# Performance work log

Measured on AMD Instinct MI355X. Metric: run time of the kernel, lower is better.

The kernel has to match this reference:

```python
import jax, jax.numpy as jnp
import numpy as np
import math

EMBED = 512
KDIM = 512
VDIM = 512
H = 8
HD = EMBED // H
N = 2048
L = 2048
B = 4


def setup_inputs() -> dict:
    key = jax.random.key(0)
    ks = jax.random.split(key, 14)
    s = 1.0 / math.sqrt(EMBED)
    return {
        "q": jax.random.normal(ks[0], (N, B, EMBED), jnp.float32),
        "k": jax.random.normal(ks[1], (L, B, KDIM), jnp.float32),
        "v": jax.random.normal(ks[2], (L, B, VDIM), jnp.float32),
        "pe1": jax.random.normal(ks[3], (B, N, 3), jnp.float32),
        "pe2": jax.random.normal(ks[4], (L, 3), jnp.float32),
        "Wq": jax.random.normal(ks[5], (EMBED, EMBED), jnp.float32) * s,
        "bq": jnp.zeros((EMBED,), jnp.float32),
        "Wk": jax.random.normal(ks[6], (EMBED, KDIM), jnp.float32) * s,
        "bk": jnp.zeros((EMBED,), jnp.float32),
        "Wv": jax.random.normal(ks[7], (EMBED, VDIM), jnp.float32) * s,
        "bv": jnp.zeros((EMBED,), jnp.float32),
        "Wo": jax.random.normal(ks[8], (EMBED, EMBED), jnp.float32) * s,
        "bo": jnp.zeros((EMBED,), jnp.float32),
    }


def reference(q, k, v, pe1, pe2, Wq, bq, Wk, bk, Wv, bv, Wo, bo):
    n, b, _ = q.shape
    l = k.shape[0]
    # projections (nn.Linear: x @ W.T + b)
    qp = q @ Wq.T + bq  # (n, b, E)
    kp = k @ Wk.T + bk  # (l, b, E)
    vp = v @ Wv.T + bv  # (l, b, E)
    # split heads -> (b, H, n, hd)
    qh = qp.reshape(n, b, H, HD).transpose(1, 2, 0, 3)
    kh = kp.reshape(l, b, H, HD).transpose(1, 2, 0, 3)
    vh = vp.reshape(l, b, H, HD).transpose(1, 2, 0, 3)
    # relative PE bias: (b, n, l), broadcast over heads
    pe_scores = jnp.einsum('bnc,lc->bnl', pe1, pe2)[:, None, :, :]
    scores = (jnp.einsum('bhnd,bhld->bhnl', qh, kh) + pe_scores) / math.sqrt(HD)
    attn = jax.nn.softmax(scores, axis=-1)
    out = jnp.einsum('bhnl,bhld->bhnd', attn, vh)  # (b, H, n, hd)
    out = out.transpose(2, 0, 1, 3).reshape(n, b, EMBED)
    return out @ Wo.T + bo
```

## Files before the change

### kernel.cpp

```cpp
#include <hip/hip_runtime.h>
#include <math.h>

#define EMBED 512
#define HDIM 64
#define NHEADS 8
#define SEQ_N 2048
#define SEQ_L 2048
#define BATCH 4
#define MROWS (SEQ_N*BATCH)
#define BE (BATCH*EMBED)

#define QSCALE 0.18033688f

typedef _Float16 f16;
typedef _Float16 half8 __attribute__((ext_vector_type(8)));
typedef _Float16 half4 __attribute__((ext_vector_type(4)));
typedef _Float16 half2v __attribute__((ext_vector_type(2)));
typedef float floatx4 __attribute__((ext_vector_type(4)));
typedef float floatx16 __attribute__((ext_vector_type(16)));

static __device__ inline float fast_exp2(float x) {
#if __has_builtin(__builtin_amdgcn_exp2f)
  return __builtin_amdgcn_exp2f(x);
#else
  return __expf(x * 0.69314718056f);
#endif
}

static __device__ inline half2v pk2(float a, float b) {
#if __has_builtin(__builtin_amdgcn_cvt_pkrtz)
  return __builtin_bit_cast(half2v, __builtin_amdgcn_cvt_pkrtz(a, b));
#else
  half2v o; o[0] = (f16)a; o[1] = (f16)b; return o;
#endif
}

static __device__ inline half8 cvt8(float4 u, float4 v) {
  half2v p0 = pk2(u.x, u.y), p1 = pk2(u.z, u.w);
  half2v p2 = pk2(v.x, v.y), p3 = pk2(v.z, v.w);
  half8 o;
  o[0] = p0[0]; o[1] = p0[1]; o[2] = p1[0]; o[3] = p1[1];
  o[4] = p2[0]; o[5] = p2[1]; o[6] = p3[0]; o[7] = p3[1];
  return o;
}

static __device__ inline void gload16(const void* g, void* l) {
  __builtin_amdgcn_global_load_lds(
      (__attribute__((address_space(1))) void*)(g),
      (__attribute__((address_space(3))) void*)(l), 16, 0, 0);
}

__global__ __launch_bounds__(256) void cvt_w(const float* __restrict__ Wq,
                                             const float* __restrict__ Wk,
                                             const float* __restrict__ Wv,
                                             const float* __restrict__ Wo,
                                             f16* __restrict__ Wb) {
  const long WSZ = (long)EMBED * EMBED;
  long i = ((long)blockIdx.x * 256 + threadIdx.x) * 4;
  int sel = (int)(i >> 18);
  long off = i & (WSZ - 1);
  const float* s = sel == 0 ? Wq : sel == 1 ? Wk : sel == 2 ? Wv : Wo;
  float4 f = *reinterpret_cast<const float4*>(s + off);
  half4 o; o[0] = (f16)f.x; o[1] = (f16)f.y; o[2] = (f16)f.z; o[3] = (f16)f.w;
  *reinterpret_cast<half4*>(Wb + i) = o;
}

__global__ __launch_bounds__(256) void gemm_qkv(const float* __restrict__ A0,
                                                const float* __restrict__ A1,
                                                const float* __restrict__ A2,
                                                const f16* __restrict__ W0,
                                                const f16* __restrict__ W1,
                                                const f16* __restrict__ W2,
                                                const float* __restrict__ b0,
                                                const float* __restrict__ b1,
                                                const float* __restrict__ b2,
                                                f16* __restrict__ C0, f16* __restrict__ C1,
                                                f16* __restrict__ C2t) {
  __shared__ alignas(16) unsigned char gsm[34816];
  f16* As = reinterpret_cast<f16*>(gsm);
  f16* Bs = reinterpret_cast<f16*>(gsm + 16384);
  f16* T  = reinterpret_cast<f16*>(gsm);
  const int sel = blockIdx.y >> 2;
  const float* A = sel == 0 ? A0 : sel == 1 ? A1 : A2;
  const f16* Bt = sel == 0 ? W0 : sel == 1 ? W1 : W2;
  const float* bias = sel == 0 ? b0 : sel == 1 ? b1 : b2;
  const float scl = sel == 0 ? QSCALE : 1.0f;
  const int tid = threadIdx.x;
  const int wave = tid >> 6, lane = tid & 63, quad = lane >> 4, l16 = lane & 15;
  const int wm = wave & 1, wn = wave >> 1;
  const long m0 = (long)blockIdx.x * 128;
  const long n0 = (long)(blockIdx.y & 3) * 128;
  const int srow = lane >> 2;
  const int scol = (lane & 3) * 8;

  const int ar = tid >> 1;
  const int ah = (tid & 1) * 16;
  const float* Agp = A + (m0 + ar) * EMBED + ah;
  const f16* Bg0 = Bt + (n0 + wave * 32 + srow) * EMBED + scol;
  const f16* Bg1 = Bt + (n0 + wave * 32 + 16 + srow) * EMBED + scol;

  {
    float4 a4[4];
#pragma unroll
    for (int j = 0; j < 4; ++j)
      a4[j] = *reinterpret_cast<const float4*>(Agp + j * 4);
    gload16(Bg0, &Bs[(wave * 32) * 32]);
    gload16(Bg1, &Bs[(wave * 32 + 16) * 32]);
    *reinterpret_cast<half8*>(&As[ar * 32 + ah]) = cvt8(a4[0], a4[1]);
    *reinterpret_cast<half8*>(&As[ar * 32 + ah + 8]) = cvt8(a4[2], a4[3]);
  }
  floatx4 acc[4][4] = {};
  __syncthreads();

#pragma unroll
  for (int ks = 0; ks < 16; ++ks) {
    const int cur = ks & 1;
    float4 a4[4];
    if (ks + 1 < 16) {
      const int k1 = (ks + 1) * 32;
#pragma unroll
      for (int j = 0; j < 4; ++j)
        a4[j] = *reinterpret_cast<const float4*>(Agp + k1 + j * 4);
      gload16(Bg0 + k1, &Bs[(cur ^ 1) * 4096 + (wave * 32) * 32]);
      gload16(Bg1 + k1, &Bs[(cur ^ 1) * 4096 + (wave * 32 + 16) * 32]);
    }
    half8 af[4], bf[4];
#pragma unroll
    for (int i = 0; i < 4; ++i)
      af[i] = *reinterpret_cast<const half8*>(&As[cur * 4096 + (wm * 64 + i * 16 + l16) * 32 + quad * 8]);
#pragma unroll
    for (int j = 0; j < 4; ++j)
      bf[j] = *reinterpret_cast<const half8*>(&Bs[cur * 4096 + (wn * 64 + j * 16 + l16) * 32 + quad * 8]);
#pragma unroll
    for (int i = 0; i < 4; ++i)
#pragma unroll
      for (int j = 0; j < 4; ++j)
        acc[i][j] = __builtin_amdgcn_mfma_f32_16x16x32_f16(af[i], bf[j], acc[i][j], 0, 0, 0);
    if (ks + 1 < 16) {
      *reinterpret_cast<half8*>(&As[(cur ^ 1) * 4096 + ar * 32 + ah]) = cvt8(a4[0], a4[1]);
      *reinterpret_cast<half8*>(&As[(cur ^ 1) * 4096 + ar * 32 + ah + 8]) = cvt8(a4[2], a4[3]);
      __syncthreads();
    }
  }

  if (sel != 2) {
    f16* C = sel == 0 ? C0 : C1;
#pragma unroll
    for (int i = 0; i < 4; ++i)
#pragma unroll
      for (int r = 0; r < 4; ++r) {
        long row = m0 + wm * 64 + i * 16 + quad * 4 + r;
#pragma unroll
        for (int j = 0; j < 4; ++j) {
          long col = n0 + wn * 64 + j * 16 + l16;
          float val = (acc[i][j][r] + bias[col]) * scl;
          C[row * EMBED + col] = (f16)val;
        }
      }
  } else {
    __syncthreads();
#pragma unroll
    for (int i = 0; i < 4; ++i)
#pragma unroll
      for (int r = 0; r < 4; ++r) {
        int mrow = wm * 64 + i * 16 + quad * 4 + r;
        int bq = mrow & 3, lt = mrow >> 2;
#pragma unroll
        for (int j = 0; j < 4; ++j) {
          int col = wn * 64 + j * 16 + l16;
          float val = acc[i][j][r] + bias[n0 + col];
          T[col * 136 + bq * 32 + lt] = (f16)val;
        }
      }
    __syncthreads();
    const int h0 = (int)(n0 >> 6);
    const long lbase = m0 >> 2;
#pragma unroll
    for (int it = 0; it < 8; ++it) {
      int f = it * 256 + tid;
      int ls = f & 3, bq = (f >> 2) & 3, d6 = (f >> 4) & 63, hl = f >> 10;
      half8 o = *reinterpret_cast<const half8*>(&T[(hl * 64 + d6) * 136 + bq * 32 + ls * 8]);
      *reinterpret_cast<half8*>(C2t + (((long)bq * 8 + h0 + hl) * 64 + d6) * 2048 + lbase + ls * 8) = o;
    }
  }
}

__global__ __launch_bounds__(256) void gemm_out(const f16* __restrict__ A,
                                                const f16* __restrict__ Bt,
                                                const float* __restrict__ bias,
                                                float* __restrict__ C) {
  __shared__ alignas(16) f16 As[2][128 * 32];
  __shared__ alignas(16) f16 Bs[2][64 * 32];
  const int tid = threadIdx.x;
  const int wave = tid >> 6, lane = tid & 63, quad = lane >> 4, l16 = lane & 15;
  const long m0 = (long)blockIdx.x * 128;
  const long n0 = (long)blockIdx.y * 64;
  const int srow = lane >> 2;
  const int scol = (lane & 3) * 8;

  const f16* Ag0 = A + (m0 + wave * 32 + srow) * EMBED + scol;
  const f16* Ag1 = A + (m0 + wave * 32 + 16 + srow) * EMBED + scol;
  const f16* Bg0 = Bt + (n0 + wave * 16 + srow) * EMBED + scol;

  gload16(Ag0, &As[0][(wave * 32) * 32]);
  gload16(Ag1, &As[0][(wave * 32 + 16) * 32]);
  gload16(Bg0, &Bs[0][(wave * 16) * 32]);
  floatx4 acc[2][4] = {};
  asm volatile("s_waitcnt vmcnt(0)" ::: "memory");
  __builtin_amdgcn_s_barrier();

#pragma unroll
  for (int ks = 0; ks < 16; ++ks) {
    const int cur = ks & 1;
    if (ks + 1 < 16) {
      const int k1 = (ks + 1) * 32;
      gload16(Ag0 + k1, &As[cur ^ 1][(wave * 32) * 32]);
      gload16(Ag1 + k1, &As[cur ^ 1][(wave * 32 + 16) * 32]);
      gload16(Bg0 + k1, &Bs[cur ^ 1][(wave * 16) * 32]);
    }
    half8 af[2], bf[4];
#pragma unroll
    for (int i = 0; i < 2; ++i)
      af[i] = *reinterpret_cast<const half8*>(&As[cur][(wave * 32 + i * 16 + l16) * 32 + quad * 8]);
#pragma unroll
    for (int j = 0; j < 4; ++j)
      bf[j] = *reinterpret_cast<const half8*>(&Bs[cur][(j * 16 + l16) * 32 + quad * 8]);
#pragma unroll
    for (int i = 0; i < 2; ++i)
#pragma unroll
      for (int j = 0; j < 4; ++j)
        acc[i][j] = __builtin_amdgcn_mfma_f32_16x16x32_f16(af[i], bf[j], acc[i][j], 0, 0, 0);
    if (ks + 1 < 16) {
      asm volatile("s_waitcnt vmcnt(0)" ::: "memory");
      __builtin_amdgcn_s_barrier();
    }
  }
#pragma unroll
  for (int i = 0; i < 2; ++i)
#pragma unroll
    for (int r = 0; r < 4; ++r) {
      long row = m0 + wave * 32 + i * 16 + quad * 4 + r;
#pragma unroll
      for (int j = 0; j < 4; ++j) {
        long col = n0 + j * 16 + l16;
        C[row * EMBED + col] = acc[i][j][r] + bias[col];
      }
    }
}

#define KBUFB (128 * 64 * 2)
#define VBUFB (64 * 128 * 2)
#define PEBUFB (128 * 16 * 2)
#define LDSB (2 * KBUFB + 2 * VBUFB + 2 * PEBUFB)
#define NCHUNK (SEQ_L / 128)
__global__ __launch_bounds__(512, 4) void attn_flash(const f16* __restrict__ qp,
                                                     const f16* __restrict__ kp,
                                                     const f16* __restrict__ vt,
                                                     const float* __restrict__ pe1,
                                                     const float* __restrict__ pe2,
                                                     f16* __restrict__ ao) {
  __shared__ alignas(16) unsigned char smem[LDSB];
  f16* K0 = reinterpret_cast<f16*>(smem);
  f16* V0 = reinterpret_cast<f16*>(smem + 2 * KBUFB);
  f16* P0 = reinterpret_cast<f16*>(smem + 2 * KBUFB + 2 * VBUFB);
  float* comb = reinterpret_cast<float*>(smem);
  const int tid = threadIdx.x, wave = tid >> 6, lane = tid & 63;
  const int m = lane & 31, h = lane >> 5;
  const int strip = wave & 3, half = wave >> 2;
  const int W = blockIdx.y * 16 + blockIdx.x;
  const int bh = (W & 7) + ((W >> 7) << 3);
  const int n0 = ((W >> 3) & 15) * 128;
  const int b = bh >> 3, hd = bh & 7;
  const long headoff = (long)b * EMBED + hd * HDIM;
  const long vhead = (long)bh * 64 * 2048;

  const int krow0 = wave * 16 + (lane >> 3);
  const int kg = (lane & 7) ^ (lane >> 3);
  const f16* ksrc0 = kp + headoff + (long)krow0 * BE + kg * 8;
  const int vd0 = wave * 8 + (lane >> 4);
  const int vd1 = vd0 + 4;
  const int vg0 = (lane & 15) ^ (vd0 & 7);
  const int vg1 = (lane & 15) ^ (vd1 & 7);
  const f16* vsrc0 = vt + vhead + (long)vd0 * 2048 + vg0 * 8;
  const f16* vsrc1 = vt + vhead + (long)vd1 * 2048 + vg1 * 8;

  for (int c = tid; c < 1024; c += 512) {
    int r = c >> 3, col = (c & 7) * 8;
    *reinterpret_cast<uint4*>(&K0[r * 64 + col]) =
        *reinterpret_cast<const uint4*>(qp + (long)(n0 + r) * BE + headoff + col);
  }
  gload16(vsrc0, V0 + wave * 1024);
  gload16(vsrc1, V0 + wave * 1024 + 512);
  if (tid < 256) {
    const uint2 z2 = {0, 0};
    const uint4 z4 = {0, 0, 0, 0};
    *reinterpret_cast<uint2*>(reinterpret_cast<char*>(P0) + tid * 32 + 8) = z2;
    *reinterpret_cast<uint4*>(reinterpret_cast<char*>(P0) + tid * 32 + 16) = z4;
  }
  if (tid < 128) {
    long base = ((long)b * SEQ_N + n0 + tid) * 3;
    half4 v8;
    v8[0] = (f16)(pe1[base + 0] * QSCALE);
    v8[1] = (f16)(pe1[base + 1] * QSCALE);
    v8[2] = (f16)(pe1[base + 2] * QSCALE);
    v8[3] = (f16)0.f;
    *reinterpret_cast<half4*>(&P0[tid * 16]) = v8;
  }
  __syncthreads();

  half8 qf[5];
#pragma unroll
  for (int e = 0; e < 4; ++e)
    qf[e] = *reinterpret_cast<const half8*>(&K0[(strip * 32 + m) * 64 + e * 16 + h * 8]);
  qf[4] = *reinterpret_cast<const half8*>(&P0[(strip * 32 + m) * 16 + h * 8]);
  __syncthreads();

  gload16(ksrc0, K0 + wave * 1024);
  gload16(ksrc0 + 8 * BE, K0 + wave * 1024 + 512);
  {
    int pr = tid & 127;
    float a0 = pe2[(long)pr * 3 + 0];
    float a1 = pe2[(long)pr * 3 + 1];
    float a2 = pe2[(long)pr * 3 + 2];
    if (tid < 128) {
      half4 p2v; p2v[0] = (f16)a0; p2v[1] = (f16)a1; p2v[2] = (f16)a2; p2v[3] = (f16)0.f;
      *reinterpret_cast<half4*>(&P0[tid * 16]) = p2v;
    }
  }
  __syncthreads();

  floatx16 oacc[2] = {};
  float lpart = 0.f;

  auto compute_chunk = [&](int bsel) {
    const f16* Kb = K0 + bsel * 8192;
    const f16* Vb = V0 + bsel * 8192;
    const f16* Pb = P0 + bsel * 2048;
#pragma unroll
    for (int tt = 0; tt < 2; ++tt) {
      const int t = half * 2 + tt;
      const int row = t * 32 + m;
      const int r7 = m & 7;
      floatx16 st = {};
#pragma unroll
      for (int e = 0; e < 4; ++e) {
        half8 kf = *reinterpret_cast<const half8*>(&Kb[row * 64 + (((2 * e + h) ^ r7) * 8)]);
        st = __builtin_amdgcn_mfma_f32_32x32x16_f16(kf, qf[e], st, 0, 0, 0);
      }
      {
        half8 kf = *reinterpret_cast<const half8*>(&Pb[row * 16 + h * 8]);
        st = __builtin_amdgcn_mfma_f32_32x32x16_f16(kf, qf[4], st, 0, 0, 0);
      }
      float p[16];
#pragma unroll
      for (int r = 0; r < 16; ++r) {
        p[r] = fast_exp2(st[r]);
        lpart += p[r];
      }
#pragma unroll
      for (int s = 0; s < 4; ++s) {
        half2v u0 = pk2(p[4 * s + 0], p[4 * s + 1]);
        half2v u1 = pk2(p[4 * s + 2], p[4 * s + 3]);
        half4 bp;
        bp[0] = u0[0]; bp[1] = u0[1]; bp[2] = u1[0]; bp[3] = u1[1];
        const int sl = t * 4 + s;
#pragma unroll
        for (int dt = 0; dt < 2; ++dt) {
          const int d = dt * 32 + m;
          half4 vf = *reinterpret_cast<const half4*>(&Vb[d * 128 + ((sl ^ r7) * 8) + h * 4]);
          oacc[dt] = __builtin_amdgcn_mfma_f32_32x32x8f16(vf, bp, oacc[dt], 0, 0, 0);
        }
      }
    }
  };

  int buf = 0;
#pragma unroll 1
  for (int c = 0; c < NCHUNK - 1; ++c) {
    const int l0n = (c + 1) * 128;
    f16* Kn = K0 + (buf ^ 1) * 8192;
    f16* Vn = V0 + (buf ^ 1) * 8192;
    gload16(ksrc0 + (long)l0n * BE, Kn + wave * 1024);
    gload16(ksrc0 + (long)l0n * BE + 8 * BE, Kn + wave * 1024 + 512);
    gload16(vsrc0 + l0n, Vn + wave * 1024);
    gload16(vsrc1 + l0n, Vn + wave * 1024 + 512);
    int pr = tid & 127;
    float a0 = pe2[(long)(l0n + pr) * 3 + 0];
    float a1 = pe2[(long)(l0n + pr) * 3 + 1];
    float a2 = pe2[(long)(l0n + pr) * 3 + 2];

    compute_chunk(buf);

    if (tid < 128) {
      half4 p2v; p2v[0] = (f16)a0; p2v[1] = (f16)a1; p2v[2] = (f16)a2; p2v[3] = (f16)0.f;
      *reinterpret_cast<half4*>(&P0[(buf ^ 1) * 2048 + tid * 16]) = p2v;
    }
    __syncthreads();
    buf ^= 1;
  }
  compute_chunk(buf);
  __syncthreads();

  lpart += __shfl_xor(lpart, 32);

  if (half == 1) {
    float* dst = comb + (strip * 64 + lane) * 33;
#pragma unroll
    for (int dt = 0; dt < 2; ++dt)
#pragma unroll
      for (int x = 0; x < 16; ++x) dst[dt * 16 + x] = oacc[dt][x];
    dst[32] = lpart;
  }
  __syncthreads();
  if (half == 0) {
    const float* src = comb + (strip * 64 + lane) * 33;
#pragma unroll
    for (int dt = 0; dt < 2; ++dt)
#pragma unroll
      for (int x = 0; x < 16; ++x) oacc[dt][x] += src[dt * 16 + x];
    float inv = 1.f / (lpart + src[32]);
    long qrow = n0 + strip * 32 + m;
#pragma unroll
    for (int dt = 0; dt < 2; ++dt)
#pragma unroll
      for (int g = 0; g < 4; ++g) {
        half4 o4;
#pragma unroll
        for (int x = 0; x < 4; ++x) o4[x] = (f16)(oacc[dt][4 * g + x] * inv);
        int d = dt * 32 + 8 * g + 4 * h;
        *reinterpret_cast<half4*>(ao + qrow * BE + headoff + d) = o4;
      }
  }
}

extern "C" void kernel_launch(void* const* d_in, const int* in_sizes, int n_in,
                              void* d_out, int out_size, void* d_ws, size_t ws_size,
                              hipStream_t stream) {
  const float* q   = (const float*)d_in[0];
  const float* k   = (const float*)d_in[1];
  const float* v   = (const float*)d_in[2];
  const float* pe1 = (const float*)d_in[3];
  const float* pe2 = (const float*)d_in[4];
  const float* Wq  = (const float*)d_in[5];
  const float* bq  = (const float*)d_in[6];
  const float* Wk  = (const float*)d_in[7];
  const float* bk  = (const float*)d_in[8];
  const float* Wv  = (const float*)d_in[9];
  const float* bv  = (const float*)d_in[10];
  const float* Wo  = (const float*)d_in[11];
  const float* bo  = (const float*)d_in[12];
  float* out = (float*)d_out;

  f16* ws = (f16*)d_ws;
  const long TOK = (long)MROWS * EMBED;
  const long WSZ = (long)EMBED * EMBED;
  f16* Wqb = ws;
  f16* Wkb = Wqb + WSZ;
  f16* Wvb = Wkb + WSZ;
  f16* Wob = Wvb + WSZ;
  f16* qpb = Wob + WSZ;
  f16* kpb = qpb + TOK;
  f16* vtb = kpb + TOK;
  f16* aob = vtb + TOK;

  cvt_w<<<dim3(1024), 256, 0, stream>>>(Wq, Wk, Wv, Wo, Wqb);

  gemm_qkv<<<dim3(MROWS / 128, 12), 256, 0, stream>>>(q, k, v, Wqb, Wkb, Wvb,
                                                      bq, bk, bv, qpb, kpb, vtb);

  attn_flash<<<dim3(SEQ_N / 128, BATCH * NHEADS), 512, 0, stream>>>(qpb, kpb, vtb, pe1, pe2, aob);

  gemm_out<<<dim3(MROWS / 128, EMBED / 64), 256, 0, stream>>>(aob, Wob, bo, out);
}
```

Baseline: 208.7 us.

## Stage fp32 A tiles via async LDS loads and use 32x32x16 MFMA for PV

The QKV projection now copies fp32 activation tiles straight into shared memory with async global-to-LDS loads, using an XOR-swizzled layout. It converts them to fp16 when it reads the MFMA fragments, so the register round trip and the separate convert-and-store step go away. In attention, the P·V product switches from 32x32x8 to 32x32x16 MFMA, using v_permlane32_swap to rearrange the packed probabilities into 8-wide fragments, which halves the MFMA instruction count. The costs are double the LDS footprint for A, which may reduce occupancy, and conversion work repeated per fragment read.

```diff
diff --git a/kernel.cpp b/kernel.cpp
--- a/kernel.cpp
+++ b/kernel.cpp
@@ -18,6 +18,7 @@
 typedef _Float16 half2v __attribute__((ext_vector_type(2)));
 typedef float floatx4 __attribute__((ext_vector_type(4)));
 typedef float floatx16 __attribute__((ext_vector_type(16)));
+typedef unsigned int uint4v __attribute__((ext_vector_type(4)));
 
 static __device__ inline float fast_exp2(float x) {
 #if __has_builtin(__builtin_amdgcn_exp2f)
@@ -76,9 +77,9 @@
                                                 const float* __restrict__ b2,
                                                 f16* __restrict__ C0, f16* __restrict__ C1,
                                                 f16* __restrict__ C2t) {
-  __shared__ alignas(16) unsigned char gsm[34816];
-  f16* As = reinterpret_cast<f16*>(gsm);
-  f16* Bs = reinterpret_cast<f16*>(gsm + 16384);
+  __shared__ alignas(16) unsigned char gsm[49152];
+  float* As = reinterpret_cast<float*>(gsm);
+  f16* Bs = reinterpret_cast<f16*>(gsm + 32768);
   f16* T  = reinterpret_cast<f16*>(gsm);
   const int sel = blockIdx.y >> 2;
   const float* A = sel == 0 ? A0 : sel == 1 ? A1 : A2;
@@ -93,41 +94,43 @@
   const int srow = lane >> 2;
   const int scol = (lane & 3) * 8;
 
-  const int ar = tid >> 1;
-  const int ah = (tid & 1) * 16;
-  const float* Agp = A + (m0 + ar) * EMBED + ah;
+  const int arow = lane >> 3;
+  const int aslot = (lane & 7) ^ arow;
+  const float* Agp = A + (m0 + wave * 32 + arow) * EMBED + aslot * 4;
   const f16* Bg0 = Bt + (n0 + wave * 32 + srow) * EMBED + scol;
   const f16* Bg1 = Bt + (n0 + wave * 32 + 16 + srow) * EMBED + scol;
 
-  {
-    float4 a4[4];
-#pragma unroll
-    for (int j = 0; j < 4; ++j)
-      a4[j] = *reinterpret_cast<const float4*>(Agp + j * 4);
-    gload16(Bg0, &Bs[(wave * 32) * 32]);
-    gload16(Bg1, &Bs[(wave * 32 + 16) * 32]);
-    *reinterpret_cast<half8*>(&As[ar * 32 + ah]) = cvt8(a4[0], a4[1]);
-    *reinterpret_cast<half8*>(&As[ar * 32 + ah + 8]) = cvt8(a4[2], a4[3]);
-  }
+#pragma unroll
+  for (int j = 0; j < 4; ++j)
+    gload16(Agp + (long)j * 8 * EMBED, As + (wave * 32 + j * 8) * 32);
+  gload16(Bg0, &Bs[(wave * 32) * 32]);
+  gload16(Bg1, &Bs[(wave * 32 + 16) * 32]);
   floatx4 acc[4][4] = {};
-  __syncthreads();
+  asm volatile("s_waitcnt vmcnt(0)" ::: "memory");
+  __builtin_amdgcn_s_barrier();
 
 #pragma unroll
   for (int ks = 0; ks < 16; ++ks) {
     const int cur = ks & 1;
-    float4 a4[4];
     if (ks + 1 < 16) {
       const int k1 = (ks + 1) * 32;
 #pragma unroll
       for (int j = 0; j < 4; ++j)
-        a4[j] = *reinterpret_cast<const float4*>(Agp + k1 + j * 4);
+        gload16(Agp + k1 + (long)j * 8 * EMBED,
+                As + (cur ^ 1) * 4096 + (wave * 32 + j * 8) * 32);
       gload16(Bg0 + k1, &Bs[(cur ^ 1) * 4096 + (wave * 32) * 32]);
       gload16(Bg1 + k1, &Bs[(cur ^ 1) * 4096 + (wave * 32 + 16) * 32]);
     }
     half8 af[4], bf[4];
 #pragma unroll
-    for (int i = 0; i < 4; ++i)
-      af[i] = *reinterpret_cast<const half8*>(&As[cur * 4096 + (wm * 64 + i * 16 + l16) * 32 + quad * 8]);
+    for (int i = 0; i < 4; ++i) {
+      const int row = wm * 64 + i * 16 + l16;
+      const int r7 = l16 & 7;
+      const float* base = As + cur * 4096 + row * 32;
+      float4 lo = *reinterpret_cast<const float4*>(base + (((quad * 2) ^ r7) * 4));
+      float4 hi = *reinterpret_cast<const float4*>(base + (((quad * 2 + 1) ^ r7) * 4));
+      af[i] = cvt8(lo, hi);
+    }
 #pragma unroll
     for (int j = 0; j < 4; ++j)
       bf[j] = *reinterpret_cast<const half8*>(&Bs[cur * 4096 + (wn * 64 + j * 16 + l16) * 32 + quad * 8]);
@@ -137,9 +140,8 @@
       for (int j = 0; j < 4; ++j)
         acc[i][j] = __builtin_amdgcn_mfma_f32_16x16x32_f16(af[i], bf[j], acc[i][j], 0, 0, 0);
     if (ks + 1 < 16) {
-      *reinterpret_cast<half8*>(&As[(cur ^ 1) * 4096 + ar * 32 + ah]) = cvt8(a4[0], a4[1]);
-      *reinterpret_cast<half8*>(&As[(cur ^ 1) * 4096 + ar * 32 + ah + 8]) = cvt8(a4[2], a4[3]);
-      __syncthreads();
+      asm volatile("s_waitcnt vmcnt(0)" ::: "memory");
+      __builtin_amdgcn_s_barrier();
     }
   }
 
@@ -358,17 +360,21 @@
         lpart += p[r];
       }
 #pragma unroll
-      for (int s = 0; s < 4; ++s) {
-        half2v u0 = pk2(p[4 * s + 0], p[4 * s + 1]);
-        half2v u1 = pk2(p[4 * s + 2], p[4 * s + 3]);
-        half4 bp;
-        bp[0] = u0[0]; bp[1] = u0[1]; bp[2] = u1[0]; bp[3] = u1[1];
-        const int sl = t * 4 + s;
+      for (int u = 0; u < 2; ++u) {
+        unsigned a0 = __builtin_bit_cast(unsigned, pk2(p[8 * u + 0], p[8 * u + 1]));
+        unsigned a1 = __builtin_bit_cast(unsigned, pk2(p[8 * u + 2], p[8 * u + 3]));
+        unsigned b0 = __builtin_bit_cast(unsigned, pk2(p[8 * u + 4], p[8 * u + 5]));
+        unsigned b1 = __builtin_bit_cast(unsigned, pk2(p[8 * u + 6], p[8 * u + 7]));
+        asm("v_permlane32_swap_b32 %0, %1" : "+v"(a0), "+v"(b0));
+        asm("v_permlane32_swap_b32 %0, %1" : "+v"(a1), "+v"(b1));
+        uint4v pkd; pkd.x = a0; pkd.y = a1; pkd.z = b0; pkd.w = b1;
+        half8 bp = __builtin_bit_cast(half8, pkd);
+        const int s8 = t * 4 + u * 2 + h;
 #pragma unroll
         for (int dt = 0; dt < 2; ++dt) {
           const int d = dt * 32 + m;
-          half4 vf = *reinterpret_cast<const half4*>(&Vb[d * 128 + ((sl ^ r7) * 8) + h * 4]);
-          oacc[dt] = __builtin_amdgcn_mfma_f32_32x32x8f16(vf, bp, oacc[dt], 0, 0, 0);
+          half8 vf = *reinterpret_cast<const half8*>(&Vb[d * 128 + ((s8 ^ r7) * 8)]);
+          oacc[dt] = __builtin_amdgcn_mfma_f32_32x32x16_f16(vf, bp, oacc[dt], 0, 0, 0);
         }
       }
     }
```

Result: faster. 195.8 us (-6.2%).
